# Optimization experiments

Measured on AMD Instinct MI355X. Metric: run time of the kernel, lower is better.

Reference implementation:

```python
import jax, jax.numpy as jnp
import numpy as np
import math

B, CIN, COUT, K, R = 8, 128, 128, 7, 2
GC = 16                     # group_channels (init arg `groups`)
G = COUT // GC              # number of dynamic-weight groups = 8
H = W = 32
EPS = 1e-5


def c4_lift(w):
    # w: [o, i, 4] -> dense 1x1 weight [o*4, i*4] via cyclic C4 shifts
    # torch: weight[:, r] = w[..., roll-by-r]  (e.g. r=1 -> [3,0,1,2])
    Wr = jnp.stack([jnp.roll(w, r, axis=-1) for r in range(4)], axis=1)  # [o,4,i,4]
    o, _, i, _ = Wr.shape
    return Wr.reshape(o * 4, i * 4)


def setup_inputs() -> dict:
    key = jax.random.key(0)
    ks = jax.random.split(key, 4)
    sc = 1.0 / math.sqrt(4 * CIN / 2)
    x = jax.random.normal(ks[0], (B, CIN * 4, H, W), dtype=jnp.float32)
    v_w = jax.random.normal(ks[1], (COUT, CIN, 4), dtype=jnp.float32) * sc
    c1_w = jax.random.normal(ks[2], (CIN // R, CIN, 4), dtype=jnp.float32) * sc
    gn_g = jnp.ones((CIN // R * 4,), jnp.float32)
    gn_b = jnp.zeros((CIN // R * 4,), jnp.float32)
    c2_w = jax.random.normal(ks[3], (K * K * G, CIN // R), dtype=jnp.float32) * (1.0 / math.sqrt(CIN // R))
    c2_b = jnp.zeros((K * K * G,), jnp.float32)
    return {"x": x, "v_w": v_w, "c1_w": c1_w, "gn_g": gn_g, "gn_b": gn_b, "c2_w": c2_w, "c2_b": c2_b}


def _forward(x, v_w, c1_w, gn_g, gn_b, c2_w, c2_b):
    b, _, h, w = x.shape
    # conv1: C4-equivariant 1x1
    t = jnp.einsum('oc,bchw->bohw', c4_lift(c1_w), x)        # [b, (CIN//R)*4, h, w]
    # GroupNorm(num_groups=CIN//R) -> normalize each group of 4 channels over (4,h,w)
    tr = t.reshape(b, CIN // R, 4, h, w)
    mu = tr.mean(axis=(2, 3, 4), keepdims=True)
    var = tr.var(axis=(2, 3, 4), keepdims=True)
    t = ((tr - mu) * jax.lax.rsqrt(var + EPS)).reshape(b, CIN // R * 4, h, w)
    t = jax.nn.relu(t * gn_g[None, :, None, None] + gn_b[None, :, None, None])
    # conv2: Conv3d 1x1 over the (c, 4) view
    tv = t.reshape(b, CIN // R, 4, h, w)
    wmap = jnp.einsum('oc,bcrhw->borhw', c2_w, tv) + c2_b[None, :, None, None, None]
    wmap = wmap.reshape(b, G, K, K, 4, h, w)
    # rotate the KxK kernel by r*90deg for C4 element r (r=0 identity)
    wmap = jnp.stack([jnp.rot90(wmap[:, :, :, :, r], k=r, axes=(2, 3)) for r in range(4)], axis=4)
    wmap = wmap.reshape(b, G, K * K, 4, h, w)                 # [b, g, p, r, h, w]
    # v branch (C4 1x1) + unfold (im2col, pad (K-1)//2, stride 1)
    v = jnp.einsum('oc,bchw->bohw', c4_lift(v_w), x)          # [b, COUT*4, h, w]
    p = (K - 1) // 2
    vp = jnp.pad(v, ((0, 0), (0, 0), (p, p), (p, p)))
    patches = jnp.stack([vp[:, :, i:i + h, j:j + w] for i in range(K) for j in range(K)], axis=2)
    patches = patches.reshape(b, G, GC, 4, K * K, h, w)       # [b, g, c, r, p, h, w]
    out = jnp.einsum('bgprhw,bgcrphw->bgcrhw', wmap, patches)
    return out.reshape(b, COUT * 4, h, w)


def reference(x, v_w, c1_w, gn_g, gn_b, c2_w, c2_b):
    return _forward(x, v_w, c1_w, gn_g, gn_b, c2_w, c2_b)
```

## Files before the change

kernel.cpp:

```cpp
#include <hip/hip_runtime.h>

#define BB   8
#define CIN  128
#define COUT 128
#define KS   7
#define HH   32
#define WWID 32
#define HW   1024
#define NG   8
#define GC   16
#define MROWS 768
#define TROWS 256
#define VROWS 512
#define KDIM 512
#define WMAP_O 392
#define WMAP_OP 448
#define C2K  64

#define AS1 __attribute__((address_space(1)))
#define AS3 __attribute__((address_space(3)))

typedef __attribute__((ext_vector_type(8))) short bf16x8;
typedef __attribute__((ext_vector_type(4))) float f32x4;

__device__ __forceinline__ short f2bf(float f) {
    unsigned u = __builtin_bit_cast(unsigned, f);
    u += 0x7fff + ((u >> 16) & 1);
    return (short)(u >> 16);
}
__device__ __forceinline__ float bf2f(unsigned short u) {
    unsigned v = (unsigned)u << 16;
    return __builtin_bit_cast(float, v);
}

__global__ __launch_bounds__(256) void prep_kernel(
    const float* __restrict__ x, const float* __restrict__ v_w,
    const float* __restrict__ c1_w, const float* __restrict__ c2_w,
    const float* __restrict__ c2_b,
    short* __restrict__ XT, short* __restrict__ Wb,
    short* __restrict__ c2wb, float* __restrict__ c2bp,
    float* __restrict__ gnstat)
{
    __shared__ short t[64][66];
    int bx = blockIdx.x, tid = threadIdx.x;
    if (bx < 1024) {
        int b = bx >> 7, c0 = ((bx >> 4) & 7) * 64, n0 = (bx & 15) * 64;
        const float* xb = x + ((size_t)b * KDIM + c0) * HW + n0;
        #pragma unroll
        for (int l = 0; l < 16; ++l) {
            int flat = l * 256 + tid;
            int row = flat >> 6, col = flat & 63;
            t[col][row] = f2bf(xb[(size_t)row * HW + col]);
        }
        __syncthreads();
        short* xt = XT + ((size_t)b * HW + n0) * KDIM + c0;
        #pragma unroll
        for (int l = 0; l < 8; ++l) {
            int u = l * 256 + tid;
            int nrow = u >> 5, cp = (u & 31) * 2;
            short2 v = make_short2(t[nrow][cp], t[nrow][cp + 1]);
            *(short2*)(xt + (size_t)nrow * KDIM + cp) = v;
        }
    } else if (bx < 2560) {
        int idx = (bx - 1024) * 256 + tid;
        int row = idx >> 9, col = idx & 511;
        int i = col >> 2, s = col & 3;
        float val;
        if (row < 256) {
            int o = row >> 2, r = row & 3;
            val = c1_w[(o * CIN + i) * 4 + ((s - r) & 3)];
        } else {
            int ro = row - 256;
            int o = ro >> 2, r = ro & 3;
            val = v_w[(o * CIN + i) * 4 + ((s - r) & 3)];
        }
        Wb[idx] = f2bf(val);
    } else if (bx < 2672) {
        int idx = (bx - 2560) * 256 + tid;
        int o = idx >> 6, k = idx & 63;
        c2wb[idx] = f2bf(o < WMAP_O ? c2_w[o * C2K + k] : 0.f);
        if (idx < WMAP_OP)
            c2bp[idx] = idx < WMAP_O ? c2_b[idx] : 0.f;
    } else {
        *(float4*)(gnstat + tid * 4) = make_float4(0.f, 0.f, 0.f, 0.f);
    }
}

#define GBM 64
#define GBN 128
#define GBK 64
__global__ __launch_bounds__(256) void gemm_mfma_kernel(
    const short* __restrict__ Wb, const short* __restrict__ XT,
    short* __restrict__ tvb, float* __restrict__ gnstat)
{
    __shared__ short As[2][GBM * GBK];
    __shared__ short Bs[2][GBN * GBK];
    int b  = blockIdx.z;
    int m0 = blockIdx.y * GBM;
    int n0 = blockIdx.x * GBN;
    int tid = threadIdx.x;
    int lane = tid & 63, wv = tid >> 6;
    int wm = wv & 1, wn = wv >> 1;
    int rl = lane & 15, kg = lane >> 4;
    const short* Ab = Wb + (size_t)m0 * KDIM;
    const short* Bb = XT + ((size_t)b * HW + n0) * KDIM;
    f32x4 acc[2][4] = {};

#define GEMM_STAGE(buf, k0)                                                              \
    do {                                                                                 \
        _Pragma("unroll")                                                                \
        for (int l = 0; l < 2; ++l) {                                                    \
            int c = l * 256 + tid;                                                       \
            int row = c >> 3, kc = c & 7;                                                \
            int kcs = kc ^ (row & 7);                                                    \
            __builtin_amdgcn_global_load_lds(                                            \
                (const AS1 void*)(Ab + (size_t)row * KDIM + (k0) + kcs * 8),             \
                (AS3 void*)(As[buf] + (l * 256 + wv * 64) * 8), 16, 0, 0);               \
        }                                                                                \
        _Pragma("unroll")                                                                \
        for (int l = 0; l < 4; ++l) {                                                    \
            int c = l * 256 + tid;                                                       \
            int row = c >> 3, kc = c & 7;                                                \
            int kcs = kc ^ (row & 7);                                                    \
            __builtin_amdgcn_global_load_lds(                                            \
                (const AS1 void*)(Bb + (size_t)row * KDIM + (k0) + kcs * 8),             \
                (AS3 void*)(Bs[buf] + (l * 256 + wv * 64) * 8), 16, 0, 0);               \
        }                                                                                \
    } while (0)

    GEMM_STAGE(0, 0);
    __syncthreads();
    for (int t = 0; t < KDIM / GBK; ++t) {
        int cur = t & 1;
        if (t < KDIM / GBK - 1) GEMM_STAGE(cur ^ 1, (t + 1) * GBK);
        #pragma unroll
        for (int ks = 0; ks < 2; ++ks) {
            bf16x8 af[2], bfr[4];
            #pragma unroll
            for (int mf = 0; mf < 2; ++mf) {
                int row = wm * 32 + mf * 16 + rl;
                af[mf] = *(const bf16x8*)(As[cur] + row * GBK + ((ks * 4 + kg) ^ (row & 7)) * 8);
            }
            #pragma unroll
            for (int nf = 0; nf < 4; ++nf) {
                int row = wn * 64 + nf * 16 + rl;
                bfr[nf] = *(const bf16x8*)(Bs[cur] + row * GBK + ((ks * 4 + kg) ^ (row & 7)) * 8);
            }
            #pragma unroll
            for (int mf = 0; mf < 2; ++mf)
                #pragma unroll
                for (int nf = 0; nf < 4; ++nf)
                    acc[mf][nf] = __builtin_amdgcn_mfma_f32_16x16x32_bf16(af[mf], bfr[nf], acc[mf][nf], 0, 0, 0);
        }
        __syncthreads();
    }
#undef GEMM_STAGE

    short* Cb = tvb + (size_t)b * MROWS * HW;
    #pragma unroll
    for (int mf = 0; mf < 2; ++mf) {
        int rowb = m0 + wm * 32 + mf * 16 + kg * 4;
        #pragma unroll
        for (int nf = 0; nf < 4; ++nf) {
            int col = n0 + wn * 64 + nf * 16 + rl;
            #pragma unroll
            for (int i = 0; i < 4; ++i)
                Cb[(size_t)(rowb + i) * HW + col] = f2bf(acc[mf][nf][i]);
        }
    }

    if (m0 < TROWS) {
        #pragma unroll
        for (int mf = 0; mf < 2; ++mf) {
            float s = 0.f, sq = 0.f;
            #pragma unroll
            for (int nf = 0; nf < 4; ++nf)
                #pragma unroll
                for (int i = 0; i < 4; ++i) {
                    float v = acc[mf][nf][i];
                    s += v; sq += v * v;
                }
            #pragma unroll
            for (int m = 1; m <= 8; m <<= 1) {
                s  += __shfl_xor(s, m);
                sq += __shfl_xor(sq, m);
            }
            if (rl == 0) {
                int grp = (m0 + wm * 32 + mf * 16 + kg * 4) >> 2;
                atomicAdd(&gnstat[(b * 64 + grp) * 2],     s);
                atomicAdd(&gnstat[(b * 64 + grp) * 2 + 1], sq);
            }
        }
    }
}

__global__ __launch_bounds__(256) void tkn2_kernel(
    const short* __restrict__ tvb, const float* __restrict__ gnstat,
    const float* __restrict__ gn_g, const float* __restrict__ gn_b,
    short* __restrict__ tn)
{
    __shared__ short ts[64][72];
    __shared__ float sc[64], sh[64];
    int b4r = blockIdx.x;
    int b = b4r >> 2, r = b4r & 3;
    int hw0 = blockIdx.y * 64;
    int tid = threadIdx.x;
    if (tid < 64) {
        float s   = gnstat[(b * 64 + tid) * 2];
        float sq  = gnstat[(b * 64 + tid) * 2 + 1];
        float mu  = s * (1.f / 4096.f);
        float var = sq * (1.f / 4096.f) - mu * mu;
        float inv = rsqrtf(var + 1e-5f);
        int ch = tid * 4 + r;
        float g = gn_g[ch], bb = gn_b[ch];
        sc[tid] = inv * g;
        sh[tid] = bb - mu * inv * g;
    }
    #pragma unroll
    for (int l = 0; l < 16; ++l) {
        int flat = l * 256 + tid;
        int c = flat >> 6, hw = flat & 63;
        ts[c][hw] = tvb[((size_t)b * MROWS + c * 4 + r) * HW + hw0 + hw];
    }
    __syncthreads();
    #pragma unroll
    for (int l = 0; l < 2; ++l) {
        int u = l * 256 + tid;
        int hw = u >> 3, c0 = (u & 7) * 8;
        bf16x8 v;
        #pragma unroll
        for (int j = 0; j < 8; ++j) {
            float f = bf2f((unsigned short)ts[c0 + j][hw]);
            f = fmaxf(f * sc[c0 + j] + sh[c0 + j], 0.f);
            v[j] = f2bf(f);
        }
        *(bf16x8*)(tn + ((size_t)b4r * HW + hw0 + hw) * C2K + c0) = v;
    }
}

__global__ __launch_bounds__(256) void wmap3_kernel(
    const short* __restrict__ c2wb, const short* __restrict__ tn,
    const float* __restrict__ c2bp, short* __restrict__ wmapB)
{
    __shared__ short smem[64 * 64 + 128 * 64];
    short* As = smem;
    short* Bs = smem + 64 * 64;
    short* Ps = smem;
    int n0  = blockIdx.x * 128;
    int m0  = blockIdx.y * 64;
    int b4r = blockIdx.z;
    int tid = threadIdx.x;
    int lane = tid & 63, wv = tid >> 6;
    int wm = wv & 1, wn = wv >> 1;
    int rl = lane & 15, kg = lane >> 4;
    const short* Bb = tn + ((size_t)b4r * HW + n0) * C2K;

    #pragma unroll
    for (int l = 0; l < 2; ++l) {
        int c = l * 256 + tid;
        int row = c >> 3, kc = c & 7;
        int kcs = kc ^ (row & 7);
        __builtin_amdgcn_global_load_lds(
            (const AS1 void*)(c2wb + (size_t)(m0 + row) * C2K + kcs * 8),
            (AS3 void*)(As + (l * 256 + wv * 64) * 8), 16, 0, 0);
    }
    #pragma unroll
    for (int l = 0; l < 4; ++l) {
        int c = l * 256 + tid;
        int row = c >> 3, kc = c & 7;
        int kcs = kc ^ (row & 7);
        __builtin_amdgcn_global_load_lds(
            (const AS1 void*)(Bb + (size_t)row * C2K + kcs * 8),
            (AS3 void*)(Bs + (l * 256 + wv * 64) * 8), 16, 0, 0);
    }
    __syncthreads();

    f32x4 acc[2][4] = {};
    #pragma unroll
    for (int ks = 0; ks < 2; ++ks) {
        bf16x8 af[2], bfr[4];
        #pragma unroll
        for (int mf = 0; mf < 2; ++mf) {
            int row = wm * 32 + mf * 16 + rl;
            af[mf] = *(const bf16x8*)(As + row * 64 + ((ks * 4 + kg) ^ (row & 7)) * 8);
        }
        #pragma unroll
        for (int nf = 0; nf < 4; ++nf) {
            int row = wn * 64 + nf * 16 + rl;
            bfr[nf] = *(const bf16x8*)(Bs + row * 64 + ((ks * 4 + kg) ^ (row & 7)) * 8);
        }
        #pragma unroll
        for (int mf = 0; mf < 2; ++mf)
            #pragma unroll
            for (int nf = 0; nf < 4; ++nf)
                acc[mf][nf] = __builtin_amdgcn_mfma_f32_16x16x32_bf16(af[mf], bfr[nf], acc[mf][nf], 0, 0, 0);
    }
    __syncthreads();

    #pragma unroll
    for (int mf = 0; mf < 2; ++mf) {
        int rowl = wm * 32 + mf * 16 + kg * 4;
        float bi[4];
        #pragma unroll
        for (int i = 0; i < 4; ++i) bi[i] = c2bp[m0 + rowl + i];
        #pragma unroll
        for (int nf = 0; nf < 4; ++nf) {
            int col = wn * 64 + nf * 16 + rl;
            #pragma unroll
            for (int i = 0; i < 4; ++i)
                Ps[(rowl + i) * 136 + col] = f2bf(acc[mf][nf][i] + bi[i]);
        }
    }
    __syncthreads();

    int row = tid >> 2, segl = tid & 3;
    if (m0 + row < WMAP_O) {
        short* dst = wmapB + (size_t)b4r * WMAP_OP * HW + (size_t)(m0 + row) * HW + n0;
        #pragma unroll
        for (int s2 = 0; s2 < 4; ++s2) {
            int col = segl * 8 + s2 * 32;
            *(bf16x8*)(dst + col) = *(const bf16x8*)(Ps + row * 136 + col);
        }
    }
}

__global__ __launch_bounds__(256, 5) void agg6_kernel(
    const short* __restrict__ tvb, const short* __restrict__ wmapB,
    float* __restrict__ out)
{
    __shared__ float vt[8][15][44];
    int bx = blockIdx.x;
    int b = bx >> 5;
    int g = (bx >> 2) & 7;
    int r = bx & 3;
    int h0   = blockIdx.y * 8;
    int half = blockIdx.z;
    int tid  = threadIdx.x;
    int w0q = tid & 7, hb = (tid >> 3) & 1, cc4 = (tid >> 4) & 3, cq = tid >> 6;
    int hl = cq * 2 + hb;
    int h = h0 + hl, w0 = w0q * 4;

    int A, Bc, Cc;
    if      (r == 0) { A = 0;  Bc = 7;  Cc = 1;  }
    else if (r == 1) { A = 6;  Bc = -1; Cc = 7;  }
    else if (r == 2) { A = 48; Bc = -7; Cc = -1; }
    else             { A = 42; Bc = 1;  Cc = -7; }

    const short* vpb = tvb + ((size_t)b * MROWS + TROWS) * HW;
    for (int e = tid; e < 8 * 15 * 3; e += 256) {
        int cc  = e / 45;
        int rem = e - cc * 45;
        int row = rem / 3, q = rem - row * 3;
        int col = (q == 0) ? 0 : (36 + (q - 1) * 4);
        *(float4*)(&vt[cc][row][col]) = make_float4(0.f, 0.f, 0.f, 0.f);
    }
    for (int f = tid; f < 8 * 15 * 8; f += 256) {
        int cc  = f / 120;
        int rem = f - cc * 120;
        int row = rem >> 3, q = rem & 7;
        int gh = h0 - 3 + row;
        float4 v4 = make_float4(0.f, 0.f, 0.f, 0.f);
        if (gh >= 0 && gh < HH) {
            int ch = (g * GC + half * 8 + cc) * 4 + r;
            ushort4 u = *(const ushort4*)(vpb + (size_t)ch * HW + gh * WWID + q * 4);
            v4 = make_float4(bf2f(u.x), bf2f(u.y), bf2f(u.z), bf2f(u.w));
        }
        *(float4*)(&vt[cc][row][4 + q * 4]) = v4;
    }
    __syncthreads();

    const short* wmb = wmapB + ((size_t)(b * 4 + r) * WMAP_OP + g * 49) * HW + h * WWID + w0;
    float acc[2][4] = {};
    #pragma unroll
    for (int di = 0; di < 7; ++di) {
        float wrf[7][4];
        #pragma unroll
        for (int dj = 0; dj < 7; ++dj) {
            int porig = A + Bc * di + Cc * dj;
            ushort4 wv = *(const ushort4*)(wmb + (size_t)porig * HW);
            wrf[dj][0] = bf2f(wv.x); wrf[dj][1] = bf2f(wv.y);
            wrf[dj][2] = bf2f(wv.z); wrf[dj][3] = bf2f(wv.w);
        }
        #pragma unroll
        for (int c2 = 0; c2 < 2; ++c2) {
            int hc = cc4 * 2 + c2;
            const float* rp = &vt[hc][hl + di][w0];
            float4 q0 = *(const float4*)(rp);
            float4 q1 = *(const float4*)(rp + 4);
            float4 q2 = *(const float4*)(rp + 8);
            float win[12] = {q0.x, q0.y, q0.z, q0.w,
                             q1.x, q1.y, q1.z, q1.w,
                             q2.x, q2.y, q2.z, q2.w};
            #pragma unroll
            for (int dj = 0; dj < 7; ++dj)
                #pragma unroll
                for (int px = 0; px < 4; ++px)
                    acc[c2][px] += wrf[dj][px] * win[px + dj + 1];
        }
    }
    #pragma unroll
    for (int c2 = 0; c2 < 2; ++c2) {
        int ch = (g * GC + half * 8 + cc4 * 2 + c2) * 4 + r;
        float4 o4 = make_float4(acc[c2][0], acc[c2][1], acc[c2][2], acc[c2][3]);
        *(float4*)(out + ((size_t)b * 512 + ch) * HW + h * WWID + w0) = o4;
    }
}

extern "C" void kernel_launch(void* const* d_in, const int* in_sizes, int n_in,
                              void* d_out, int out_size, void* d_ws, size_t ws_size,
                              hipStream_t stream)
{
    const float* x    = (const float*)d_in[0];
    const float* v_w  = (const float*)d_in[1];
    const float* c1_w = (const float*)d_in[2];
    const float* gn_g = (const float*)d_in[3];
    const float* gn_b = (const float*)d_in[4];
    const float* c2_w = (const float*)d_in[5];
    const float* c2_b = (const float*)d_in[6];
    float* out = (float*)d_out;

    char* p = (char*)d_ws;
    short* Wb     = (short*)p;           p += (size_t)MROWS * KDIM * 2;
    short* tvb    = (short*)p;           p += (size_t)BB * MROWS * HW * 2;
    short* wmapB  = (short*)p;           p += (size_t)32 * WMAP_OP * HW * 2;
    short* XT     = (short*)wmapB;
    short* tn     = (short*)p;           p += (size_t)32 * HW * C2K * 2;
    short* c2wb   = (short*)p;           p += (size_t)WMAP_OP * C2K * 2;
    float* c2bp   = (float*)p;           p += (size_t)WMAP_OP * 4;
    float* gnstat = (float*)p;           p += (size_t)512 * 2 * 4;

    prep_kernel     <<<2673, 256, 0, stream>>>(x, v_w, c1_w, c2_w, c2_b, XT, Wb, c2wb, c2bp, gnstat);
    gemm_mfma_kernel<<<dim3(HW / GBN, MROWS / GBM, BB), 256, 0, stream>>>(Wb, XT, tvb, gnstat);
    tkn2_kernel     <<<dim3(32, 16), 256, 0, stream>>>(tvb, gnstat, gn_g, gn_b, tn);
    wmap3_kernel    <<<dim3(HW / 128, WMAP_OP / 64, 32), 256, 0, stream>>>(c2wb, tn, c2bp, wmapB);
    agg6_kernel     <<<dim3(BB * NG * 4, 4, 2), 256, 0, stream>>>(tvb, wmapB, out);
}
```

Measured before the change: 61.36 us.

## Fuse GroupNorm+ReLU transpose kernel into the wmap GEMM

Merges the separate normalize/transpose kernel into the conv2 GEMM kernel. Each block now loads its tile of tvb, applies GroupNorm scale/shift and ReLU in shared memory, and writes the swizzled B tile directly. This drops the tn intermediate buffer round trip and one kernel launch. The N tile is halved to 64 to match. In exchange, each normalized tile is recomputed by all 7 M-blocks, and the GEMM work per block is smaller.

```diff
diff --git a/kernel.cpp b/kernel.cpp
--- a/kernel.cpp
+++ b/kernel.cpp
@@ -194,17 +194,37 @@
     }
 }
 
-__global__ __launch_bounds__(256) void tkn2_kernel(
-    const short* __restrict__ tvb, const float* __restrict__ gnstat,
-    const float* __restrict__ gn_g, const float* __restrict__ gn_b,
-    short* __restrict__ tn)
+__global__ __launch_bounds__(256) void wmap4_kernel(
+    const short* __restrict__ c2wb, const short* __restrict__ tvb,
+    const float* __restrict__ gnstat, const float* __restrict__ gn_g,
+    const float* __restrict__ gn_b, const float* __restrict__ c2bp,
+    short* __restrict__ wmapB)
 {
-    __shared__ short ts[64][72];
+    __shared__ short smem[4096 + 4096 + 4608];
     __shared__ float sc[64], sh[64];
-    int b4r = blockIdx.x;
+    short* As = smem;
+    short* Bs = smem + 4096;
+    short* T  = smem + 8192;
+    short* Ps = smem;
+
+    int n0  = blockIdx.x * 64;
+    int m0  = blockIdx.y * 64;
+    int b4r = blockIdx.z;
     int b = b4r >> 2, r = b4r & 3;
-    int hw0 = blockIdx.y * 64;
     int tid = threadIdx.x;
+    int lane = tid & 63, wv = tid >> 6;
+    int wm = wv & 1, wn = (wv >> 1) & 1;
+    int rl = lane & 15, kg = lane >> 4;
+
+    #pragma unroll
+    for (int l = 0; l < 2; ++l) {
+        int c = l * 256 + tid;
+        int row = c >> 3, kc = c & 7;
+        int kcs = kc ^ (row & 7);
+        __builtin_amdgcn_global_load_lds(
+            (const AS1 void*)(c2wb + (size_t)(m0 + row) * C2K + kcs * 8),
+            (AS3 void*)(As + (l * 256 + wv * 64) * 8), 16, 0, 0);
+    }
     if (tid < 64) {
         float s   = gnstat[(b * 64 + tid) * 2];
         float sq  = gnstat[(b * 64 + tid) * 2 + 1];
@@ -212,87 +232,54 @@
         float var = sq * (1.f / 4096.f) - mu * mu;
         float inv = rsqrtf(var + 1e-5f);
         int ch = tid * 4 + r;
-        float g = gn_g[ch], bb = gn_b[ch];
+        float g = gn_g[ch], bb2 = gn_b[ch];
         sc[tid] = inv * g;
-        sh[tid] = bb - mu * inv * g;
-    }
-    #pragma unroll
-    for (int l = 0; l < 16; ++l) {
-        int flat = l * 256 + tid;
-        int c = flat >> 6, hw = flat & 63;
-        ts[c][hw] = tvb[((size_t)b * MROWS + c * 4 + r) * HW + hw0 + hw];
-    }
-    __syncthreads();
+        sh[tid] = bb2 - mu * inv * g;
+    }
     #pragma unroll
     for (int l = 0; l < 2; ++l) {
-        int u = l * 256 + tid;
-        int hw = u >> 3, c0 = (u & 7) * 8;
+        int cid = l * 256 + tid;
+        int c = cid >> 3, ch = cid & 7;
+        bf16x8 v = *(const bf16x8*)(tvb + ((size_t)b * MROWS + c * 4 + r) * HW + n0 + ch * 8);
+        *(bf16x8*)(T + c * 72 + ch * 8) = v;
+    }
+    __syncthreads();
+
+    #pragma unroll
+    for (int l = 0; l < 2; ++l) {
+        int cid = l * 256 + tid;
+        int row = cid >> 3, kc = cid & 7;
+        int kcs = kc ^ (row & 7);
         bf16x8 v;
         #pragma unroll
         for (int j = 0; j < 8; ++j) {
-            float f = bf2f((unsigned short)ts[c0 + j][hw]);
-            f = fmaxf(f * sc[c0 + j] + sh[c0 + j], 0.f);
+            int c = kc * 8 + j;
+            float f = bf2f((unsigned short)T[c * 72 + row]);
+            f = fmaxf(f * sc[c] + sh[c], 0.f);
             v[j] = f2bf(f);
         }
-        *(bf16x8*)(tn + ((size_t)b4r * HW + hw0 + hw) * C2K + c0) = v;
-    }
-}
-
-__global__ __launch_bounds__(256) void wmap3_kernel(
-    const short* __restrict__ c2wb, const short* __restrict__ tn,
-    const float* __restrict__ c2bp, short* __restrict__ wmapB)
-{
-    __shared__ short smem[64 * 64 + 128 * 64];
-    short* As = smem;
-    short* Bs = smem + 64 * 64;
-    short* Ps = smem;
-    int n0  = blockIdx.x * 128;
-    int m0  = blockIdx.y * 64;
-    int b4r = blockIdx.z;
-    int tid = threadIdx.x;
-    int lane = tid & 63, wv = tid >> 6;
-    int wm = wv & 1, wn = wv >> 1;
-    int rl = lane & 15, kg = lane >> 4;
-    const short* Bb = tn + ((size_t)b4r * HW + n0) * C2K;
-
-    #pragma unroll
-    for (int l = 0; l < 2; ++l) {
-        int c = l * 256 + tid;
-        int row = c >> 3, kc = c & 7;
-        int kcs = kc ^ (row & 7);
-        __builtin_amdgcn_global_load_lds(
-            (const AS1 void*)(c2wb + (size_t)(m0 + row) * C2K + kcs * 8),
-            (AS3 void*)(As + (l * 256 + wv * 64) * 8), 16, 0, 0);
-    }
-    #pragma unroll
-    for (int l = 0; l < 4; ++l) {
-        int c = l * 256 + tid;
-        int row = c >> 3, kc = c & 7;
-        int kcs = kc ^ (row & 7);
-        __builtin_amdgcn_global_load_lds(
-            (const AS1 void*)(Bb + (size_t)row * C2K + kcs * 8),
-            (AS3 void*)(Bs + (l * 256 + wv * 64) * 8), 16, 0, 0);
-    }
-    __syncthreads();
-
-    f32x4 acc[2][4] = {};
+        *(bf16x8*)(Bs + row * 64 + kcs * 8) = v;
+    }
+    __syncthreads();
+
+    f32x4 acc[2][2] = {};
     #pragma unroll
     for (int ks = 0; ks < 2; ++ks) {
-        bf16x8 af[2], bfr[4];
+        bf16x8 af[2], bfr[2];
         #pragma unroll
         for (int mf = 0; mf < 2; ++mf) {
             int row = wm * 32 + mf * 16 + rl;
             af[mf] = *(const bf16x8*)(As + row * 64 + ((ks * 4 + kg) ^ (row & 7)) * 8);
         }
         #pragma unroll
-        for (int nf = 0; nf < 4; ++nf) {
-            int row = wn * 64 + nf * 16 + rl;
+        for (int nf = 0; nf < 2; ++nf) {
+            int row = wn * 32 + nf * 16 + rl;
             bfr[nf] = *(const bf16x8*)(Bs + row * 64 + ((ks * 4 + kg) ^ (row & 7)) * 8);
         }
         #pragma unroll
         for (int mf = 0; mf < 2; ++mf)
             #pragma unroll
-            for (int nf = 0; nf < 4; ++nf)
+            for (int nf = 0; nf < 2; ++nf)
                 acc[mf][nf] = __builtin_amdgcn_mfma_f32_16x16x32_bf16(af[mf], bfr[nf], acc[mf][nf], 0, 0, 0);
     }
     __syncthreads();
@@ -304,11 +291,11 @@
         #pragma unroll
         for (int i = 0; i < 4; ++i) bi[i] = c2bp[m0 + rowl + i];
         #pragma unroll
-        for (int nf = 0; nf < 4; ++nf) {
-            int col = wn * 64 + nf * 16 + rl;
+        for (int nf = 0; nf < 2; ++nf) {
+            int col = wn * 32 + nf * 16 + rl;
             #pragma unroll
             for (int i = 0; i < 4; ++i)
-                Ps[(rowl + i) * 136 + col] = f2bf(acc[mf][nf][i] + bi[i]);
+                Ps[(rowl + i) * 68 + col] = f2bf(acc[mf][nf][i] + bi[i]);
         }
     }
     __syncthreads();
@@ -317,9 +304,9 @@
     if (m0 + row < WMAP_O) {
         short* dst = wmapB + (size_t)b4r * WMAP_OP * HW + (size_t)(m0 + row) * HW + n0;
         #pragma unroll
-        for (int s2 = 0; s2 < 4; ++s2) {
+        for (int s2 = 0; s2 < 2; ++s2) {
             int col = segl * 8 + s2 * 32;
-            *(bf16x8*)(dst + col) = *(const bf16x8*)(Ps + row * 136 + col);
+            *(bf16x8*)(dst + col) = *(const bf16x8*)(Ps + row * 68 + col);
         }
     }
 }
@@ -424,14 +411,12 @@
     short* tvb    = (short*)p;           p += (size_t)BB * MROWS * HW * 2;
     short* wmapB  = (short*)p;           p += (size_t)32 * WMAP_OP * HW * 2;
     short* XT     = (short*)wmapB;
-    short* tn     = (short*)p;           p += (size_t)32 * HW * C2K * 2;
     short* c2wb   = (short*)p;           p += (size_t)WMAP_OP * C2K * 2;
     float* c2bp   = (float*)p;           p += (size_t)WMAP_OP * 4;
     float* gnstat = (float*)p;           p += (size_t)512 * 2 * 4;
 
     prep_kernel     <<<2673, 256, 0, stream>>>(x, v_w, c1_w, c2_w, c2_b, XT, Wb, c2wb, c2bp, gnstat);
     gemm_mfma_kernel<<<dim3(HW / GBN, MROWS / GBM, BB), 256, 0, stream>>>(Wb, XT, tvb, gnstat);
-    tkn2_kernel     <<<dim3(32, 16), 256, 0, stream>>>(tvb, gnstat, gn_g, gn_b, tn);
-    wmap3_kernel    <<<dim3(HW / 128, WMAP_OP / 64, 32), 256, 0, stream>>>(c2wb, tn, c2bp, wmapB);
+    wmap4_kernel    <<<dim3(16, 7, 32), 256, 0, stream>>>(c2wb, tvb, gnstat, gn_g, gn_b, c2bp, wmapB);
     agg6_kernel     <<<dim3(BB * NG * 4, 4, 2), 256, 0, stream>>>(tvb, wmapB, out);
 }
```

Result: slower. 67.66 us (+10.3%).
